# Optimization experiments

Hardware: AMD Instinct MI355X
Metric: run time of the kernel (lower is better)

The kernel has to match this reference:

```python
import jax, jax.numpy as jnp
import numpy as np

B, S, D, H = 4, 2048, 1024, 16
HD = D // H
EPS = 1e-5


def gelu_tanh(x):
    c = jnp.sqrt(jnp.asarray(2.0 / jnp.pi, x.dtype))
    return x * 0.5 * (1.0 + jnp.tanh(c * (x + 0.044715 * x ** 3)))


def layer_norm(x, scale, shift):
    mean = jnp.mean(x, axis=-1, keepdims=True)
    var = jnp.var(x, axis=-1, keepdims=True)  # unbiased=False
    return scale * ((x - mean) / jnp.sqrt(var + EPS)) + shift


def setup_inputs() -> dict:
    key = jax.random.key(0)
    ks = jax.random.split(key, 8)
    s = 0.02
    return {
        "x": jax.random.normal(ks[0], (B, S, D), jnp.float32),
        "Wqkv": jax.random.normal(ks[1], (D, 3 * D), jnp.float32) * s,
        "Wout": jax.random.normal(ks[2], (D, D), jnp.float32) * s,
        "bout": jnp.zeros((D,), jnp.float32),
        "W1": jax.random.normal(ks[3], (D, 4 * D), jnp.float32) * s,
        "b1": jnp.zeros((4 * D,), jnp.float32),
        "W2": jax.random.normal(ks[4], (4 * D, D), jnp.float32) * s,
        "b2": jnp.zeros((D,), jnp.float32),
        "g1": jnp.ones((D,), jnp.float32),
        "s1": jnp.zeros((D,), jnp.float32),
        "g2": jnp.ones((D,), jnp.float32),
        "s2": jnp.zeros((D,), jnp.float32),
    }


def reference(x, Wqkv, Wout, bout, W1, b1, W2, b2, g1, s1, g2, s2):
    # --- attention branch ---
    h = layer_norm(x, g1, s1)
    qkv = h @ Wqkv  # [B,S,3D]
    qkv = qkv.reshape(B, S, 3, H, HD).transpose(2, 0, 3, 1, 4)  # [3,B,H,S,hd]
    q, k, v = qkv[0], qkv[1], qkv[2]
    scores = jnp.einsum("bhqd,bhkd->bhqk", q, k)
    causal = jnp.triu(jnp.ones((S, S), bool), k=1)
    scores = jnp.where(causal, -jnp.inf, scores)
    attn = jax.nn.softmax(scores / jnp.sqrt(jnp.asarray(HD, x.dtype)), axis=-1)
    ctx = jnp.einsum("bhqk,bhkd->bhqd", attn, v)
    ctx = ctx.transpose(0, 2, 1, 3).reshape(B, S, D)
    x = x + (ctx @ Wout + bout)
    # --- MLP branch ---
    h = layer_norm(x, g2, s2)
    h = gelu_tanh(h @ W1 + b1) @ W2 + b2
    return x + h
```

## Files before the change

### kernel.cpp

```cpp
#include <hip/hip_runtime.h>
#include <stdint.h>

typedef unsigned short u16;
typedef unsigned long long u64;
typedef __attribute__((ext_vector_type(8))) short bf16x8;
typedef __attribute__((ext_vector_type(4))) float f32x4;

#define DEV __device__ __forceinline__

DEV u16 f2bf(float f) {
  union { float f; unsigned u; } v; v.f = f;
  unsigned r = (v.u + 0x7fffu + ((v.u >> 16) & 1u)) >> 16;
  return (u16)r;
}

#define GLDS(g, l) __builtin_amdgcn_global_load_lds( \
    (const __attribute__((address_space(1))) void*)(g), \
    (__attribute__((address_space(3))) void*)(l), 16, 0, 0)

__global__ __launch_bounds__(256) void k_transpose_cast(
    const float* __restrict__ in, u16* __restrict__ out, int K, int N) {
  __shared__ float tile[32][33];
  int bx = blockIdx.x, by = blockIdx.y;
  int tx = threadIdx.x & 31, ty = threadIdx.x >> 5;
#pragma unroll
  for (int r = 0; r < 32; r += 8)
    tile[ty + r][tx] = in[(size_t)(by * 32 + ty + r) * N + bx * 32 + tx];
  __syncthreads();
#pragma unroll
  for (int r = 0; r < 32; r += 8)
    out[(size_t)(bx * 32 + ty + r) * K + by * 32 + tx] = f2bf(tile[tx][ty + r]);
}

__global__ __launch_bounds__(256) void k_layernorm(
    const float* __restrict__ x, const float* __restrict__ gamma,
    const float* __restrict__ beta, u16* __restrict__ out) {
  int row = blockIdx.x, t = threadIdx.x;
  const float4 v = ((const float4*)(x + (size_t)row * 1024))[t];
  float sum = v.x + v.y + v.z + v.w;
  float sq = v.x * v.x + v.y * v.y + v.z * v.z + v.w * v.w;
#pragma unroll
  for (int o = 32; o >= 1; o >>= 1) {
    sum += __shfl_down(sum, o);
    sq += __shfl_down(sq, o);
  }
  __shared__ float red[8];
  if ((t & 63) == 0) { red[(t >> 6) * 2] = sum; red[(t >> 6) * 2 + 1] = sq; }
  __syncthreads();
  sum = red[0] + red[2] + red[4] + red[6];
  sq = red[1] + red[3] + red[5] + red[7];
  float mean = sum * (1.0f / 1024.0f);
  float var = sq * (1.0f / 1024.0f) - mean * mean;
  float rstd = rsqrtf(var + 1e-5f);
  float4 g = ((const float4*)gamma)[t];
  float4 b = ((const float4*)beta)[t];
  ushort4 o4;
  o4.x = f2bf(g.x * (v.x - mean) * rstd + b.x);
  o4.y = f2bf(g.y * (v.y - mean) * rstd + b.y);
  o4.z = f2bf(g.z * (v.z - mean) * rstd + b.z);
  o4.w = f2bf(g.w * (v.w - mean) * rstd + b.w);
  ((ushort4*)(out + (size_t)row * 1024))[t] = o4;
}

struct EpiQKV {
  u16 *Q, *K2, *VT;
  DEV void operator()(int r, int c0, const f32x4& v) const {
    int three = c0 >> 10, h = (c0 >> 6) & 15, hd = c0 & 63;
    int b = r >> 11, s = r & 2047;
    int bh = b * 16 + h;
    ushort4 o;
    o.x = f2bf(v[0]); o.y = f2bf(v[1]); o.z = f2bf(v[2]); o.w = f2bf(v[3]);
    if (three == 0)
      *(ushort4*)&Q[((size_t)bh * 2048 + s) * 64 + hd] = o;
    else if (three == 1)
      *(ushort4*)&K2[((size_t)bh * 2048 + s) * 64 + hd] = o;
    else {
      VT[((size_t)bh * 64 + hd + 0) * 2048 + s] = o.x;
      VT[((size_t)bh * 64 + hd + 1) * 2048 + s] = o.y;
      VT[((size_t)bh * 64 + hd + 2) * 2048 + s] = o.z;
      VT[((size_t)bh * 64 + hd + 3) * 2048 + s] = o.w;
    }
  }
};

struct EpiBiasResid {
  const float* bias; const float* resid; float* out; int N;
  DEV void operator()(int r, int c0, const f32x4& v) const {
    size_t idx = (size_t)r * N + c0;
    float4 bb = *(const float4*)&bias[c0];
    float4 rr = *(const float4*)&resid[idx];
    float4 o;
    o.x = v[0] + bb.x + rr.x; o.y = v[1] + bb.y + rr.y;
    o.z = v[2] + bb.z + rr.z; o.w = v[3] + bb.w + rr.w;
    *(float4*)&out[idx] = o;
  }
};

struct EpiBiasGelu {
  const float* bias; u16* out; int N;
  DEV float gelu(float xx) const {
    float u = 0.7978845608f * (xx + 0.044715f * xx * xx * xx);
    float e = __expf(2.0f * u);
    float th = 1.0f - 2.0f / (e + 1.0f);
    return 0.5f * xx * (1.0f + th);
  }
  DEV void operator()(int r, int c0, const f32x4& v) const {
    float4 bb = *(const float4*)&bias[c0];
    ushort4 o;
    o.x = f2bf(gelu(v[0] + bb.x)); o.y = f2bf(gelu(v[1] + bb.y));
    o.z = f2bf(gelu(v[2] + bb.z)); o.w = f2bf(gelu(v[3] + bb.w));
    *(ushort4*)&out[(size_t)r * N + c0] = o;
  }
};

template <typename Epi>
__global__ __launch_bounds__(256) void k_gemm_tn(
    const u16* __restrict__ A, const u16* __restrict__ Bt, int K, Epi epi) {
  __shared__ u16 As[128 * 32];
  __shared__ u16 Bs[128 * 32];
  const int t = threadIdx.x;
  const int bm = blockIdx.x, bn = blockIdx.y;
  const int lane = t & 63, w = t >> 6;
  const int wm = w >> 1, wn = w & 1;
  const int quad = lane >> 4, l16 = lane & 15;
  f32x4 acc[4][4] = {};
  const u16* gA = A + (size_t)(bm * 128 + (t >> 2)) * K + (t & 3) * 8;
  const u16* gB = Bt + (size_t)(bn * 128 + (t >> 2)) * K + (t & 3) * 8;
  u16* lA = &As[t * 8];
  u16* lB = &Bs[t * 8];
  for (int k0 = 0; k0 < K; k0 += 32) {
    __syncthreads();
    GLDS(gA, lA);
    GLDS(gA + (size_t)64 * K, lA + 2048);
    GLDS(gB, lB);
    GLDS(gB + (size_t)64 * K, lB + 2048);
    gA += 32; gB += 32;
    __syncthreads();
    bf16x8 af[4], bfr[4];
#pragma unroll
    for (int mt = 0; mt < 4; ++mt)
      af[mt] = *(const bf16x8*)&As[(wm * 64 + mt * 16 + l16) * 32 + quad * 8];
#pragma unroll
    for (int nt = 0; nt < 4; ++nt)
      bfr[nt] = *(const bf16x8*)&Bs[(wn * 64 + nt * 16 + l16) * 32 + quad * 8];
#pragma unroll
    for (int mt = 0; mt < 4; ++mt)
#pragma unroll
      for (int nt = 0; nt < 4; ++nt)
        acc[mt][nt] = __builtin_amdgcn_mfma_f32_16x16x32_bf16(
            bfr[nt], af[mt], acc[mt][nt], 0, 0, 0);
  }
  const int r0 = bm * 128 + wm * 64 + l16;
  const int c0 = bn * 128 + wn * 64 + quad * 4;
#pragma unroll
  for (int mt = 0; mt < 4; ++mt)
#pragma unroll
    for (int nt = 0; nt < 4; ++nt)
      epi(r0 + mt * 16, c0 + nt * 16, acc[mt][nt]);
}

#define PW 72

__global__ __launch_bounds__(256) void k_attn(
    const u16* __restrict__ Qg, const u16* __restrict__ Kg,
    const u16* __restrict__ VTg, u16* __restrict__ ctx) {
  const int bh = blockIdx.x;
  const int qt = 31 - blockIdx.y;
  const int b = bh >> 4, h = bh & 15;
  const int t = threadIdx.x, lane = t & 63, w = t >> 6;
  const int quad = lane >> 4, l16 = lane & 15;
  const int q0 = qt * 64;
  __shared__ u16 Qs[64 * PW], Ks[64 * PW], Vs[64 * PW];
  __shared__ u16 Ps[4][16 * PW];
  __shared__ float l_lds[4][16];
  const u16* Qbase = Qg + (size_t)bh * (2048 * 64);
  const u16* Kbase = Kg + (size_t)bh * (2048 * 64);
  const u16* Vbase = VTg + (size_t)bh * (64 * 2048);
#pragma unroll
  for (int j = 0; j < 4; ++j) {
    int ch = t + 256 * j, r = ch >> 4, cc = (ch & 15) * 4;
    *(u64*)&Qs[r * PW + cc] = *(const u64*)(Qbase + (size_t)(q0 + r) * 64 + cc);
  }
  __syncthreads();
  bf16x8 qf0 = *(const bf16x8*)&Qs[(w * 16 + l16) * PW + quad * 8];
  bf16x8 qf1 = *(const bf16x8*)&Qs[(w * 16 + l16) * PW + 32 + quad * 8];
  const int qrow = q0 + w * 16 + l16;
  const float c1 = 0.18033688011f;
  float lsum = 0.f;
  f32x4 acco[4] = {};
  for (int kt = 0; kt <= qt; ++kt) {
    const int k0 = kt * 64;
    __syncthreads();
#pragma unroll
    for (int j = 0; j < 4; ++j) {
      int ch = t + 256 * j, r = ch >> 4, cc = (ch & 15) * 4;
      *(u64*)&Ks[r * PW + cc] =
          *(const u64*)(Kbase + (size_t)(k0 + r) * 64 + cc);
      *(u64*)&Vs[r * PW + cc] =
          *(const u64*)(Vbase + (size_t)r * 2048 + k0 + cc);
    }
    __syncthreads();
    f32x4 sacc[4] = {};
#pragma unroll
    for (int kk = 0; kk < 2; ++kk) {
      bf16x8 qf = kk ? qf1 : qf0;
#pragma unroll
      for (int nt = 0; nt < 4; ++nt) {
        bf16x8 kf = *(const bf16x8*)&Ks[(nt * 16 + l16) * PW + kk * 32 + quad * 8];
        sacc[nt] = __builtin_amdgcn_mfma_f32_16x16x32_bf16(kf, qf, sacc[nt], 0, 0, 0);
      }
    }
    const bool diag = (kt == qt);
    float ls = 0.f;
#pragma unroll
    for (int nt = 0; nt < 4; ++nt) {
      ushort4 o;
#pragma unroll
      for (int reg = 0; reg < 4; ++reg) {
        float p = __builtin_amdgcn_exp2f(sacc[nt][reg] * c1);
        if (diag && (k0 + nt * 16 + quad * 4 + reg > qrow)) p = 0.f;
        ls += p;
        (&o.x)[reg] = f2bf(p);
      }
      *(ushort4*)&Ps[w][l16 * PW + nt * 16 + quad * 4] = o;
    }
    ls += __shfl_xor(ls, 16);
    ls += __shfl_xor(ls, 32);
    lsum += ls;
#pragma unroll
    for (int kk = 0; kk < 2; ++kk) {
      bf16x8 pf = *(const bf16x8*)&Ps[w][l16 * PW + kk * 32 + quad * 8];
#pragma unroll
      for (int nt = 0; nt < 4; ++nt) {
        bf16x8 vf = *(const bf16x8*)&Vs[(nt * 16 + l16) * PW + kk * 32 + quad * 8];
        acco[nt] = __builtin_amdgcn_mfma_f32_16x16x32_bf16(pf, vf, acco[nt], 0, 0, 0);
      }
    }
  }
  if (quad == 0) l_lds[w][l16] = lsum;
  float4 lv = *(const float4*)&l_lds[w][quad * 4];
  float inv[4];
  inv[0] = 1.0f / lv.x; inv[1] = 1.0f / lv.y;
  inv[2] = 1.0f / lv.z; inv[3] = 1.0f / lv.w;
#pragma unroll
  for (int nt = 0; nt < 4; ++nt)
#pragma unroll
    for (int reg = 0; reg < 4; ++reg) {
      float o = acco[nt][reg] * inv[reg];
      int q = q0 + w * 16 + quad * 4 + reg;
      ctx[((size_t)(b * 2048 + q)) * 1024 + h * 64 + nt * 16 + l16] = f2bf(o);
    }
}

extern "C" void kernel_launch(void* const* d_in, const int* in_sizes, int n_in,
                              void* d_out, int out_size, void* d_ws, size_t ws_size,
                              hipStream_t stream) {
  (void)in_sizes; (void)n_in; (void)out_size; (void)ws_size;
  const float* x    = (const float*)d_in[0];
  const float* Wqkv = (const float*)d_in[1];
  const float* Wout = (const float*)d_in[2];
  const float* bout = (const float*)d_in[3];
  const float* W1   = (const float*)d_in[4];
  const float* b1   = (const float*)d_in[5];
  const float* W2   = (const float*)d_in[6];
  const float* b2   = (const float*)d_in[7];
  const float* g1   = (const float*)d_in[8];
  const float* s1   = (const float*)d_in[9];
  const float* g2   = (const float*)d_in[10];
  const float* s2   = (const float*)d_in[11];

  char* ws = (char*)d_ws;
  u16*   WqkvT = (u16*)(ws + 0);
  u16*   WoutT = (u16*)(ws + 6291456);
  u16*   W1T   = (u16*)(ws + 8388608);
  u16*   W2T   = (u16*)(ws + 16777216);
  float* x1    = (float*)(ws + 25165824);
  u16*   h12   = (u16*)(ws + 58720256);
  u16*   Qb    = (u16*)(ws + 75497472);
  u16*   Kb    = (u16*)(ws + 92274688);
  u16*   VTb   = (u16*)(ws + 109051904);
  u16*   ctx   = (u16*)(ws + 125829120);
  u16*   a1    = (u16*)(ws + 75497472);

  k_transpose_cast<<<dim3(96, 32), 256, 0, stream>>>(Wqkv, WqkvT, 1024, 3072);
  k_transpose_cast<<<dim3(32, 32), 256, 0, stream>>>(Wout, WoutT, 1024, 1024);
  k_transpose_cast<<<dim3(128, 32), 256, 0, stream>>>(W1, W1T, 1024, 4096);
  k_transpose_cast<<<dim3(32, 128), 256, 0, stream>>>(W2, W2T, 4096, 1024);

  k_layernorm<<<8192, 256, 0, stream>>>(x, g1, s1, h12);
  k_gemm_tn<<<dim3(64, 24), 256, 0, stream>>>(h12, WqkvT, 1024,
                                              EpiQKV{Qb, Kb, VTb});
  k_attn<<<dim3(64, 32), 256, 0, stream>>>(Qb, Kb, VTb, ctx);
  k_gemm_tn<<<dim3(64, 8), 256, 0, stream>>>(ctx, WoutT, 1024,
                                             EpiBiasResid{bout, x, x1, 1024});
  k_layernorm<<<8192, 256, 0, stream>>>(x1, g2, s2, h12);
  k_gemm_tn<<<dim3(64, 32), 256, 0, stream>>>(h12, W1T, 1024,
                                              EpiBiasGelu{b1, a1, 4096});
  k_gemm_tn<<<dim3(64, 8), 256, 0, stream>>>(a1, W2T, 4096,
                                             EpiBiasResid{b2, x1, (float*)d_out, 1024});
}
```

Baseline: 559.2 us.

## Process K=64 per GEMM iteration and merge weight transposes into one launch

The GEMM main loop now stages two 32-wide K slices into separate LDS buffers per iteration, halving the number of barrier pairs and putting more global loads in flight per sync. The four weight transpose-cast launches are combined into one kernel that picks its matrix from the block index, cutting launch overhead. LDS usage per GEMM block doubles, which may lower occupancy.

```diff
diff --git a/kernel.cpp b/kernel.cpp
--- a/kernel.cpp
+++ b/kernel.cpp
@@ -18,10 +18,19 @@
     (const __attribute__((address_space(1))) void*)(g), \
     (__attribute__((address_space(3))) void*)(l), 16, 0, 0)
 
-__global__ __launch_bounds__(256) void k_transpose_cast(
-    const float* __restrict__ in, u16* __restrict__ out, int K, int N) {
+__global__ __launch_bounds__(256) void k_transpose_all(
+    const float* __restrict__ Wqkv, const float* __restrict__ Wout,
+    const float* __restrict__ W1, const float* __restrict__ W2,
+    u16* __restrict__ WqkvT, u16* __restrict__ WoutT,
+    u16* __restrict__ W1T, u16* __restrict__ W2T) {
+  int id = blockIdx.x;
+  const float* in; u16* out; int K, N, nx, base;
+  if (id < 3072)      { in = Wqkv; out = WqkvT; K = 1024; N = 3072; nx = 96;  base = 0; }
+  else if (id < 4096) { in = Wout; out = WoutT; K = 1024; N = 1024; nx = 32;  base = 3072; }
+  else if (id < 8192) { in = W1;   out = W1T;   K = 1024; N = 4096; nx = 128; base = 4096; }
+  else                { in = W2;   out = W2T;   K = 4096; N = 1024; nx = 32;  base = 8192; }
+  int seg = id - base, bx = seg % nx, by = seg / nx;
   __shared__ float tile[32][33];
-  int bx = blockIdx.x, by = blockIdx.y;
   int tx = threadIdx.x & 31, ty = threadIdx.x >> 5;
 #pragma unroll
   for (int r = 0; r < 32; r += 8)
@@ -116,8 +125,8 @@
 template <typename Epi>
 __global__ __launch_bounds__(256) void k_gemm_tn(
     const u16* __restrict__ A, const u16* __restrict__ Bt, int K, Epi epi) {
-  __shared__ u16 As[128 * 32];
-  __shared__ u16 Bs[128 * 32];
+  __shared__ u16 As[2][128 * 32];
+  __shared__ u16 Bs[2][128 * 32];
   const int t = threadIdx.x;
   const int bm = blockIdx.x, bn = blockIdx.y;
   const int lane = t & 63, w = t >> 6;
@@ -126,29 +135,32 @@
   f32x4 acc[4][4] = {};
   const u16* gA = A + (size_t)(bm * 128 + (t >> 2)) * K + (t & 3) * 8;
   const u16* gB = Bt + (size_t)(bn * 128 + (t >> 2)) * K + (t & 3) * 8;
-  u16* lA = &As[t * 8];
-  u16* lB = &Bs[t * 8];
-  for (int k0 = 0; k0 < K; k0 += 32) {
+  u16* lA0 = &As[0][t * 8]; u16* lA1 = &As[1][t * 8];
+  u16* lB0 = &Bs[0][t * 8]; u16* lB1 = &Bs[1][t * 8];
+  for (int k0 = 0; k0 < K; k0 += 64) {
     __syncthreads();
-    GLDS(gA, lA);
-    GLDS(gA + (size_t)64 * K, lA + 2048);
-    GLDS(gB, lB);
-    GLDS(gB + (size_t)64 * K, lB + 2048);
-    gA += 32; gB += 32;
+    GLDS(gA, lA0);      GLDS(gA + (size_t)64 * K, lA0 + 2048);
+    GLDS(gA + 32, lA1); GLDS(gA + 32 + (size_t)64 * K, lA1 + 2048);
+    GLDS(gB, lB0);      GLDS(gB + (size_t)64 * K, lB0 + 2048);
+    GLDS(gB + 32, lB1); GLDS(gB + 32 + (size_t)64 * K, lB1 + 2048);
+    gA += 64; gB += 64;
     __syncthreads();
-    bf16x8 af[4], bfr[4];
-#pragma unroll
-    for (int mt = 0; mt < 4; ++mt)
-      af[mt] = *(const bf16x8*)&As[(wm * 64 + mt * 16 + l16) * 32 + quad * 8];
-#pragma unroll
-    for (int nt = 0; nt < 4; ++nt)
-      bfr[nt] = *(const bf16x8*)&Bs[(wn * 64 + nt * 16 + l16) * 32 + quad * 8];
-#pragma unroll
-    for (int mt = 0; mt < 4; ++mt)
+#pragma unroll
+    for (int kk = 0; kk < 2; ++kk) {
+      bf16x8 af[4], bfr[4];
+#pragma unroll
+      for (int mt = 0; mt < 4; ++mt)
+        af[mt] = *(const bf16x8*)&As[kk][(wm * 64 + mt * 16 + l16) * 32 + quad * 8];
 #pragma unroll
       for (int nt = 0; nt < 4; ++nt)
-        acc[mt][nt] = __builtin_amdgcn_mfma_f32_16x16x32_bf16(
-            bfr[nt], af[mt], acc[mt][nt], 0, 0, 0);
+        bfr[nt] = *(const bf16x8*)&Bs[kk][(wn * 64 + nt * 16 + l16) * 32 + quad * 8];
+#pragma unroll
+      for (int mt = 0; mt < 4; ++mt)
+#pragma unroll
+        for (int nt = 0; nt < 4; ++nt)
+          acc[mt][nt] = __builtin_amdgcn_mfma_f32_16x16x32_bf16(
+              bfr[nt], af[mt], acc[mt][nt], 0, 0, 0);
+    }
   }
   const int r0 = bm * 128 + wm * 64 + l16;
   const int c0 = bn * 128 + wn * 64 + quad * 4;
@@ -282,10 +294,8 @@
   u16*   ctx   = (u16*)(ws + 125829120);
   u16*   a1    = (u16*)(ws + 75497472);
 
-  k_transpose_cast<<<dim3(96, 32), 256, 0, stream>>>(Wqkv, WqkvT, 1024, 3072);
-  k_transpose_cast<<<dim3(32, 32), 256, 0, stream>>>(Wout, WoutT, 1024, 1024);
-  k_transpose_cast<<<dim3(128, 32), 256, 0, stream>>>(W1, W1T, 1024, 4096);
-  k_transpose_cast<<<dim3(32, 128), 256, 0, stream>>>(W2, W2T, 4096, 1024);
+  k_transpose_all<<<12288, 256, 0, stream>>>(Wqkv, Wout, W1, W2,
+                                             WqkvT, WoutT, W1T, W2T);
 
   k_layernorm<<<8192, 256, 0, stream>>>(x, g1, s1, h12);
   k_gemm_tn<<<dim3(64, 24), 256, 0, stream>>>(h12, WqkvT, 1024,
```

Result: faster. 531.0 us (-5.0%).

## Remap GEMM/attention blocks per XCD, async-load attention tiles, merge transposes

Applied to the files above, without the earlier changes.

GEMM and attention blocks now use a 1D grid, with block ids remapped so that each XCD (id&7) works on a contiguous group of N-columns or heads. This is meant to improve L2 reuse of shared B tiles and K/V within a chiplet. Attention Q/K/V tiles are now loaded with global_load_lds directly into an unpadded split-K layout, replacing register-staged stores into padded rows. That may add LDS bank conflicts on the fragment reads. The four weight transpose launches are merged into a single launch.

```diff
diff --git a/kernel.cpp b/kernel.cpp
--- a/kernel.cpp
+++ b/kernel.cpp
@@ -18,10 +18,19 @@
     (const __attribute__((address_space(1))) void*)(g), \
     (__attribute__((address_space(3))) void*)(l), 16, 0, 0)
 
-__global__ __launch_bounds__(256) void k_transpose_cast(
-    const float* __restrict__ in, u16* __restrict__ out, int K, int N) {
+__global__ __launch_bounds__(256) void k_transpose_all(
+    const float* __restrict__ Wqkv, const float* __restrict__ Wout,
+    const float* __restrict__ W1, const float* __restrict__ W2,
+    u16* __restrict__ WqkvT, u16* __restrict__ WoutT,
+    u16* __restrict__ W1T, u16* __restrict__ W2T) {
+  int id = blockIdx.x;
+  const float* in; u16* out; int K, N, nx, base;
+  if (id < 3072)      { in = Wqkv; out = WqkvT; K = 1024; N = 3072; nx = 96;  base = 0; }
+  else if (id < 4096) { in = Wout; out = WoutT; K = 1024; N = 1024; nx = 32;  base = 3072; }
+  else if (id < 8192) { in = W1;   out = W1T;   K = 1024; N = 4096; nx = 128; base = 4096; }
+  else                { in = W2;   out = W2T;   K = 4096; N = 1024; nx = 32;  base = 8192; }
+  int seg = id - base, bx = seg % nx, by = seg / nx;
   __shared__ float tile[32][33];
-  int bx = blockIdx.x, by = blockIdx.y;
   int tx = threadIdx.x & 31, ty = threadIdx.x >> 5;
 #pragma unroll
   for (int r = 0; r < 32; r += 8)
@@ -119,7 +128,11 @@
   __shared__ u16 As[128 * 32];
   __shared__ u16 Bs[128 * 32];
   const int t = threadIdx.x;
-  const int bm = blockIdx.x, bn = blockIdx.y;
+  const int id = blockIdx.x;
+  const int nbn8 = gridDim.x >> 9;
+  const int xcd = id & 7, slot = id >> 3;
+  const int bm = slot & 63;
+  const int bn = xcd * nbn8 + (slot >> 6);
   const int lane = t & 63, w = t >> 6;
   const int wm = w >> 1, wn = w & 1;
   const int quad = lane >> 4, l16 = lane & 15;
@@ -164,26 +177,28 @@
 __global__ __launch_bounds__(256) void k_attn(
     const u16* __restrict__ Qg, const u16* __restrict__ Kg,
     const u16* __restrict__ VTg, u16* __restrict__ ctx) {
-  const int bh = blockIdx.x;
-  const int qt = 31 - blockIdx.y;
+  const int id = blockIdx.x;
+  const int xcd = id & 7, slot = id >> 3;
+  const int bh = xcd * 8 + (slot >> 5);
+  const int qt = 31 - (slot & 31);
   const int b = bh >> 4, h = bh & 15;
   const int t = threadIdx.x, lane = t & 63, w = t >> 6;
   const int quad = lane >> 4, l16 = lane & 15;
   const int q0 = qt * 64;
-  __shared__ u16 Qs[64 * PW], Ks[64 * PW], Vs[64 * PW];
+  __shared__ u16 Qs[2 * 2048], Ks[2 * 2048], Vs[2 * 2048];
   __shared__ u16 Ps[4][16 * PW];
   __shared__ float l_lds[4][16];
   const u16* Qbase = Qg + (size_t)bh * (2048 * 64);
   const u16* Kbase = Kg + (size_t)bh * (2048 * 64);
   const u16* Vbase = VTg + (size_t)bh * (64 * 2048);
-#pragma unroll
-  for (int j = 0; j < 4; ++j) {
-    int ch = t + 256 * j, r = ch >> 4, cc = (ch & 15) * 4;
-    *(u64*)&Qs[r * PW + cc] = *(const u64*)(Qbase + (size_t)(q0 + r) * 64 + cc);
+  {
+    const u16* g = Qbase + (size_t)(q0 + (t >> 2)) * 64 + (t & 3) * 8;
+    GLDS(g, &Qs[t * 8]);
+    GLDS(g + 32, &Qs[2048 + t * 8]);
   }
   __syncthreads();
-  bf16x8 qf0 = *(const bf16x8*)&Qs[(w * 16 + l16) * PW + quad * 8];
-  bf16x8 qf1 = *(const bf16x8*)&Qs[(w * 16 + l16) * PW + 32 + quad * 8];
+  bf16x8 qf0 = *(const bf16x8*)&Qs[(w * 16 + l16) * 32 + quad * 8];
+  bf16x8 qf1 = *(const bf16x8*)&Qs[2048 + (w * 16 + l16) * 32 + quad * 8];
   const int qrow = q0 + w * 16 + l16;
   const float c1 = 0.18033688011f;
   float lsum = 0.f;
@@ -191,13 +206,13 @@
   for (int kt = 0; kt <= qt; ++kt) {
     const int k0 = kt * 64;
     __syncthreads();
-#pragma unroll
-    for (int j = 0; j < 4; ++j) {
-      int ch = t + 256 * j, r = ch >> 4, cc = (ch & 15) * 4;
-      *(u64*)&Ks[r * PW + cc] =
-          *(const u64*)(Kbase + (size_t)(k0 + r) * 64 + cc);
-      *(u64*)&Vs[r * PW + cc] =
-          *(const u64*)(Vbase + (size_t)r * 2048 + k0 + cc);
+    {
+      const u16* gk = Kbase + (size_t)(k0 + (t >> 2)) * 64 + (t & 3) * 8;
+      GLDS(gk, &Ks[t * 8]);
+      GLDS(gk + 32, &Ks[2048 + t * 8]);
+      const u16* gv = Vbase + (size_t)(t >> 2) * 2048 + k0 + (t & 3) * 8;
+      GLDS(gv, &Vs[t * 8]);
+      GLDS(gv + 32, &Vs[2048 + t * 8]);
     }
     __syncthreads();
     f32x4 sacc[4] = {};
@@ -206,7 +221,7 @@
       bf16x8 qf = kk ? qf1 : qf0;
 #pragma unroll
       for (int nt = 0; nt < 4; ++nt) {
-        bf16x8 kf = *(const bf16x8*)&Ks[(nt * 16 + l16) * PW + kk * 32 + quad * 8];
+        bf16x8 kf = *(const bf16x8*)&Ks[kk * 2048 + (nt * 16 + l16) * 32 + quad * 8];
         sacc[nt] = __builtin_amdgcn_mfma_f32_16x16x32_bf16(kf, qf, sacc[nt], 0, 0, 0);
       }
     }
@@ -232,7 +247,7 @@
       bf16x8 pf = *(const bf16x8*)&Ps[w][l16 * PW + kk * 32 + quad * 8];
 #pragma unroll
       for (int nt = 0; nt < 4; ++nt) {
-        bf16x8 vf = *(const bf16x8*)&Vs[(nt * 16 + l16) * PW + kk * 32 + quad * 8];
+        bf16x8 vf = *(const bf16x8*)&Vs[kk * 2048 + (nt * 16 + l16) * 32 + quad * 8];
         acco[nt] = __builtin_amdgcn_mfma_f32_16x16x32_bf16(pf, vf, acco[nt], 0, 0, 0);
       }
     }
@@ -282,20 +297,18 @@
   u16*   ctx   = (u16*)(ws + 125829120);
   u16*   a1    = (u16*)(ws + 75497472);
 
-  k_transpose_cast<<<dim3(96, 32), 256, 0, stream>>>(Wqkv, WqkvT, 1024, 3072);
-  k_transpose_cast<<<dim3(32, 32), 256, 0, stream>>>(Wout, WoutT, 1024, 1024);
-  k_transpose_cast<<<dim3(128, 32), 256, 0, stream>>>(W1, W1T, 1024, 4096);
-  k_transpose_cast<<<dim3(32, 128), 256, 0, stream>>>(W2, W2T, 4096, 1024);
+  k_transpose_all<<<12288, 256, 0, stream>>>(Wqkv, Wout, W1, W2,
+                                             WqkvT, WoutT, W1T, W2T);
 
   k_layernorm<<<8192, 256, 0, stream>>>(x, g1, s1, h12);
-  k_gemm_tn<<<dim3(64, 24), 256, 0, stream>>>(h12, WqkvT, 1024,
-                                              EpiQKV{Qb, Kb, VTb});
-  k_attn<<<dim3(64, 32), 256, 0, stream>>>(Qb, Kb, VTb, ctx);
-  k_gemm_tn<<<dim3(64, 8), 256, 0, stream>>>(ctx, WoutT, 1024,
-                                             EpiBiasResid{bout, x, x1, 1024});
+  k_gemm_tn<<<1536, 256, 0, stream>>>(h12, WqkvT, 1024,
+                                      EpiQKV{Qb, Kb, VTb});
+  k_attn<<<2048, 256, 0, stream>>>(Qb, Kb, VTb, ctx);
+  k_gemm_tn<<<512, 256, 0, stream>>>(ctx, WoutT, 1024,
+                                     EpiBiasResid{bout, x, x1, 1024});
   k_layernorm<<<8192, 256, 0, stream>>>(x1, g2, s2, h12);
-  k_gemm_tn<<<dim3(64, 32), 256, 0, stream>>>(h12, W1T, 1024,
-                                              EpiBiasGelu{b1, a1, 4096});
-  k_gemm_tn<<<dim3(64, 8), 256, 0, stream>>>(a1, W2T, 4096,
-                                             EpiBiasResid{b2, x1, (float*)d_out, 1024});
-}
+  k_gemm_tn<<<2048, 256, 0, stream>>>(h12, W1T, 1024,
+                                      EpiBiasGelu{b1, a1, 4096});
+  k_gemm_tn<<<512, 256, 0, stream>>>(a1, W2T, 4096,
+                                     EpiBiasResid{b2, x1, (float*)d_out, 1024});
+}
```

New measurement: 587.2 us. 5.0% more time.
